# Kernel tuning notes

Measured on AMD Instinct MI355X. Metric: run time of the kernel, lower is better.

Reference implementation:

```python
import jax, jax.numpy as jnp
import numpy as np

FEAT_DIM = 2048
HID = 256
N = 1024
NUM_CLASSES = 16
BN_EPS = 1e-5


def _batchnorm(x, gamma, beta):
    # training-mode BatchNorm1d: per-batch mean, biased variance
    m = x.mean(axis=0)
    v = x.var(axis=0)
    return gamma * (x - m) / jnp.sqrt(v + BN_EPS) + beta


def setup_inputs() -> dict:
    key = jax.random.key(0)
    ks = jax.random.split(key, 12)
    s1 = 1.0 / np.sqrt(FEAT_DIM)
    s2 = 1.0 / np.sqrt(HID)
    s3 = 1.0 / np.sqrt(2 * HID)
    return {
        "features": jax.random.normal(ks[0], (N, FEAT_DIM), dtype=jnp.float32),
        "labels": jax.random.randint(ks[1], (N,), 0, NUM_CLASSES, dtype=jnp.int32),
        # semantic disentangler
        "W1": jax.random.normal(ks[2], (FEAT_DIM, HID), dtype=jnp.float32) * s1,
        "b1": jnp.zeros((HID,), jnp.float32),
        "g1": jnp.ones((HID,), jnp.float32),
        "bt1": jnp.zeros((HID,), jnp.float32),
        "W2": jax.random.normal(ks[3], (HID, HID), dtype=jnp.float32) * s2,
        "b2": jnp.zeros((HID,), jnp.float32),
        "g2": jnp.ones((HID,), jnp.float32),
        "bt2": jnp.zeros((HID,), jnp.float32),
        # edge network: Linear(2H -> H), Linear(H -> 1)
        "We1": jax.random.normal(ks[4], (2 * HID, HID), dtype=jnp.float32) * s3,
        "bwe1": jnp.zeros((HID,), jnp.float32),
        "We2": jax.random.normal(ks[5], (HID, 1), dtype=jnp.float32) * s2,
        "bwe2": jnp.zeros((1,), jnp.float32),
    }


def reference(features, labels, W1, b1, g1, bt1, W2, b2, g2, bt2,
              We1, bwe1, We2, bwe2):
    # semantic disentangler: (Linear -> BN -> ReLU) x2
    h = jax.nn.relu(_batchnorm(features @ W1 + b1, g1, bt1))
    di = jax.nn.relu(_batchnorm(h @ W2 + b2, g2, bt2))  # [N, H]

    # EdgeNetwork all-pairs: Linear on concat([f_i, f_j]) splits into two GEMMs
    hi = di @ We1[:HID]   # [N, H] contribution of node i (first half of concat)
    hj = di @ We1[HID:]   # [N, H] contribution of node j (second half)
    pair = jax.nn.relu(hi[:, None, :] + hj[None, :, :] + bwe1)  # [N, N, H]
    logits = pair @ We2[:, 0] + bwe2[0]                          # [N, N]
    same_label = labels[:, None] == labels[None, :]
    off_diag = ~jnp.eye(N, dtype=bool)
    edge_weights = jnp.where(same_label & off_diag,
                             jax.nn.sigmoid(logits), 0.0)        # [N, N]

    # update_node_features: f_i + sum_j w_ij f_j / sum_j w_ij (if wsum > 0)
    weighted_sum = edge_weights @ di                 # [N, H] (w_ii == 0)
    wsum = edge_weights.sum(axis=1, keepdims=True)   # [N, 1]
    denom = jnp.where(wsum > 0, wsum, 1.0)
    updated = di + jnp.where(wsum > 0, weighted_sum / denom, 0.0)
    return updated
```

## Files before the change

kernel.cpp:

```cpp
#include <hip/hip_runtime.h>
#include <math.h>

#define N_PTS 1024
#define HID   256
#define FEAT  2048

typedef short bf16x8 __attribute__((ext_vector_type(8)));
typedef float f32x4  __attribute__((ext_vector_type(4)));

__device__ inline ushort f2bf(float f) {
    union { float f; unsigned u; } v; v.f = f;
    unsigned r = v.u + 0x7fff + ((v.u >> 16) & 1);
    return (ushort)(r >> 16);
}

__global__ __launch_bounds__(256) void gemm_mfma(
    const float* __restrict__ A, const float* __restrict__ B,
    float* __restrict__ C, int lda, int ldb, int ldc, int kchunk)
{
    __shared__ ushort As[64 * 72];
    __shared__ ushort Bs[64 * 72];
    const int tid  = threadIdx.x;
    const int lane = tid & 63;
    const int wave = tid >> 6;
    const int wy = wave >> 1, wx = wave & 1;
    const int quad = lane >> 4, l16 = lane & 15;
    const int mBase = blockIdx.y * 64;
    const int nBase = blockIdx.x * 64;
    const int kBeg  = blockIdx.z * kchunk;

    f32x4 acc[2][2] = {};

    for (int ks = kBeg; ks < kBeg + kchunk; ks += 64) {
        #pragma unroll
        for (int p = 0; p < 4; p++) {
            const int c  = p * 256 + tid;
            const int r  = c >> 4;
            const int cq = c & 15;
            float4 av = *(const float4*)&A[(size_t)(mBase + r) * lda + ks + cq * 4];
            ushort4 ao;
            ao.x = f2bf(av.x); ao.y = f2bf(av.y);
            ao.z = f2bf(av.z); ao.w = f2bf(av.w);
            *(ushort4*)&As[r * 72 + cq * 4] = ao;
            float4 bv = *(const float4*)&B[(size_t)(ks + r) * ldb + nBase + cq * 4];
            Bs[(cq * 4 + 0) * 72 + r] = f2bf(bv.x);
            Bs[(cq * 4 + 1) * 72 + r] = f2bf(bv.y);
            Bs[(cq * 4 + 2) * 72 + r] = f2bf(bv.z);
            Bs[(cq * 4 + 3) * 72 + r] = f2bf(bv.w);
        }
        __syncthreads();
        #pragma unroll
        for (int kt = 0; kt < 64; kt += 32) {
            bf16x8 af[2], bfr[2];
            #pragma unroll
            for (int mi = 0; mi < 2; mi++)
                af[mi] = *(bf16x8*)&As[(wy * 32 + mi * 16 + l16) * 72 + kt + quad * 8];
            #pragma unroll
            for (int ni = 0; ni < 2; ni++)
                bfr[ni] = *(bf16x8*)&Bs[(wx * 32 + ni * 16 + l16) * 72 + kt + quad * 8];
            #pragma unroll
            for (int mi = 0; mi < 2; mi++)
                #pragma unroll
                for (int ni = 0; ni < 2; ni++)
                    acc[mi][ni] = __builtin_amdgcn_mfma_f32_16x16x32_bf16(
                        af[mi], bfr[ni], acc[mi][ni], 0, 0, 0);
        }
        __syncthreads();
    }
    #pragma unroll
    for (int mi = 0; mi < 2; mi++)
        #pragma unroll
        for (int ni = 0; ni < 2; ni++)
            #pragma unroll
            for (int e = 0; e < 4; e++) {
                const int gm = mBase + wy * 32 + mi * 16 + quad * 4 + e;
                const int gn = nBase + wx * 32 + ni * 16 + l16;
                unsafeAtomicAdd(&C[(size_t)gm * ldc + gn], acc[mi][ni][e]);
            }
}

__global__ __launch_bounds__(256) void colstats(
    const float* __restrict__ X, float* __restrict__ sum,
    float* __restrict__ sq, int rowsPerBlock)
{
    const int c = threadIdx.x;
    const int r0 = blockIdx.x * rowsPerBlock;
    float s = 0.f, q = 0.f;
    for (int r = r0; r < r0 + rowsPerBlock; ++r) {
        float v = X[r * HID + c];
        s += v;
        q = fmaf(v, v, q);
    }
    unsafeAtomicAdd(&sum[c], s);
    unsafeAtomicAdd(&sq[c], q);
}

__global__ __launch_bounds__(256) void bn_relu(
    const float* __restrict__ X, const float* __restrict__ sum,
    const float* __restrict__ sq, const float* __restrict__ g,
    const float* __restrict__ bt, float* __restrict__ Y)
{
    const int idx = blockIdx.x * 256 + threadIdx.x;
    const int cq = (idx & 63) * 4;
    float4 x = ((const float4*)X)[idx];
    float xv[4] = {x.x, x.y, x.z, x.w};
    float o[4];
    #pragma unroll
    for (int e = 0; e < 4; e++) {
        const int c = cq + e;
        float m   = sum[c] * (1.f / 1024.f);
        float var = fmaf(-m, m, sq[c] * (1.f / 1024.f));
        float rstd = rsqrtf(var + 1e-5f);
        o[e] = fmaxf(fmaf(g[c] * rstd, xv[e] - m, bt[c]), 0.f);
    }
    ((float4*)Y)[idx] = make_float4(o[0], o[1], o[2], o[3]);
}

__global__ __launch_bounds__(256) void pair_update(
    const float* __restrict__ di, const float* __restrict__ hi,
    const float* __restrict__ hj, const float* __restrict__ bwe1,
    const float* __restrict__ We2, const float* __restrict__ bwe2,
    const int* __restrict__ labels, float* __restrict__ out)
{
    __shared__ int   slab[N_PTS];
    __shared__ float sacc[4][HID];
    __shared__ float swsum[4];
    const int i = blockIdx.x;
    const int tid = threadIdx.x;
    const int lane = tid & 63;
    const int wave = tid >> 6;

    for (int t = tid; t < N_PTS; t += 256) slab[t] = labels[t];
    __syncthreads();

    const int myLab = slab[i];
    float4 hv_i = ((const float4*)(hi + (size_t)i * HID))[lane];
    float4 bw   = ((const float4*)bwe1)[lane];
    float4 w2   = ((const float4*)We2)[lane];
    const float hb0 = hv_i.x + bw.x, hb1 = hv_i.y + bw.y;
    const float hb2 = hv_i.z + bw.z, hb3 = hv_i.w + bw.w;
    const float b2 = bwe2[0];

    float a0 = 0.f, a1 = 0.f, a2 = 0.f, a3 = 0.f, wsum = 0.f;

    for (int chunk = wave * 64; chunk < N_PTS; chunk += 256) {
        const int j = chunk + lane;
        const bool match = (slab[j] == myLab) && (j != i);
        unsigned long long mask = __ballot(match);
        while (mask) {
            const int bpos = __builtin_ctzll(mask);
            mask &= mask - 1;
            const int jj = chunk + bpos;
            float4 hv = ((const float4*)(hj + (size_t)jj * HID))[lane];
            float p = fmaxf(hb0 + hv.x, 0.f) * w2.x
                    + fmaxf(hb1 + hv.y, 0.f) * w2.y
                    + fmaxf(hb2 + hv.z, 0.f) * w2.z
                    + fmaxf(hb3 + hv.w, 0.f) * w2.w;
            #pragma unroll
            for (int off = 1; off < 64; off <<= 1) p += __shfl_xor(p, off, 64);
            const float w = 1.f / (1.f + expf(-(p + b2)));
            float4 dv = ((const float4*)(di + (size_t)jj * HID))[lane];
            a0 = fmaf(w, dv.x, a0);
            a1 = fmaf(w, dv.y, a1);
            a2 = fmaf(w, dv.z, a2);
            a3 = fmaf(w, dv.w, a3);
            wsum += w;
        }
    }
    ((float4*)sacc[wave])[lane] = make_float4(a0, a1, a2, a3);
    if (lane == 0) swsum[wave] = wsum;
    __syncthreads();

    const float at = sacc[0][tid] + sacc[1][tid] + sacc[2][tid] + sacc[3][tid];
    const float wt = swsum[0] + swsum[1] + swsum[2] + swsum[3];
    const float dval = di[(size_t)i * HID + tid];
    out[(size_t)i * HID + tid] = dval + (wt > 0.f ? at / wt : 0.f);
}

extern "C" void kernel_launch(void* const* d_in, const int* in_sizes, int n_in,
                              void* d_out, int out_size, void* d_ws, size_t ws_size,
                              hipStream_t stream)
{
    const float* features = (const float*)d_in[0];
    const int*   labels   = (const int*)d_in[1];
    const float* W1   = (const float*)d_in[2];
    const float* g1   = (const float*)d_in[4];
    const float* bt1  = (const float*)d_in[5];
    const float* W2   = (const float*)d_in[6];
    const float* g2   = (const float*)d_in[8];
    const float* bt2  = (const float*)d_in[9];
    const float* We1  = (const float*)d_in[10];
    const float* bwe1 = (const float*)d_in[11];
    const float* We2  = (const float*)d_in[12];
    const float* bwe2 = (const float*)d_in[13];
    float* out = (float*)d_out;

    float* ws    = (float*)d_ws;
    float* x1    = ws;
    float* x2    = ws + 262144;
    float* hi    = ws + 524288;
    float* hj    = ws + 786432;
    float* stats = ws + 1048576;
    float* h     = ws + 1049600;
    float* di    = ws + 1311744;

    hipMemsetAsync(d_ws, 0, 1049600 * sizeof(float), stream);

    dim3 blk(256);
    gemm_mfma<<<dim3(4, 16, 8), blk, 0, stream>>>(features, W1, x1,
                                                  FEAT, HID, HID, 256);
    colstats<<<256, blk, 0, stream>>>(x1, stats, stats + 256, 4);
    bn_relu<<<256, blk, 0, stream>>>(x1, stats, stats + 256, g1, bt1, h);
    gemm_mfma<<<dim3(4, 16, 4), blk, 0, stream>>>(h, W2, x2,
                                                  HID, HID, HID, 64);
    colstats<<<256, blk, 0, stream>>>(x2, stats + 512, stats + 768, 4);
    bn_relu<<<256, blk, 0, stream>>>(x2, stats + 512, stats + 768, g2, bt2, di);
    gemm_mfma<<<dim3(4, 16, 4), blk, 0, stream>>>(di, We1, hi,
                                                  HID, HID, HID, 64);
    gemm_mfma<<<dim3(4, 16, 4), blk, 0, stream>>>(di, We1 + HID * HID, hj,
                                                  HID, HID, HID, 64);
    pair_update<<<N_PTS, blk, 0, stream>>>(di, hi, hj, bwe1, We2, bwe2,
                                           labels, out);
}
```

Measured before the change: 160.6 us.

## Fuse BN1 into GEMM2 with stats epilogue, merge edge GEMMs, restructure pair kernel

Folds the first BN+ReLU into the A-tile load of the second GEMM and computes column statistics for the second BN in that GEMM's epilogue. This removes the intermediate h buffer, one colstats launch, and the split-K atomics. The two edge GEMMs become a single launch, and the memset shrinks. The pair kernel now builds a compacted list of matching neighbours in shared memory and processes 16 pairs at once with 16-lane groups, replacing the per-match 64-lane reductions and giving more parallel work per block.

Measured after the change: 155.1 us. -3.4%, faster.

```diff
diff --git a/kernel.cpp b/kernel.cpp
--- a/kernel.cpp
+++ b/kernel.cpp
@@ -116,63 +116,258 @@
     ((float4*)Y)[idx] = make_float4(o[0], o[1], o[2], o[3]);
 }
 
-__global__ __launch_bounds__(256) void pair_update(
+__global__ __launch_bounds__(256) void gemm2_fused(
+    const float* __restrict__ A , const float* __restrict__ B ,
+    float* __restrict__ C ,
+    const float* __restrict__ sum1, const float* __restrict__ sq1,
+    const float* __restrict__ g1, const float* __restrict__ bt1,
+    float* __restrict__ sum2, float* __restrict__ sq2)
+{
+    __shared__ ushort As[64 * 72];
+    __shared__ ushort Bs[64 * 72];
+    __shared__ float sscale[HID];
+    __shared__ float sshift[HID];
+    __shared__ float csum[64];
+    __shared__ float csq[64];
+    const int tid  = threadIdx.x;
+    const int lane = tid & 63;
+    const int wave = tid >> 6;
+    const int wy = wave >> 1, wx = wave & 1;
+    const int quad = lane >> 4, l16 = lane & 15;
+    const int mBase = blockIdx.y * 64;
+    const int nBase = blockIdx.x * 64;
+
+    {
+        float m   = sum1[tid] * (1.f / 1024.f);
+        float var = fmaf(-m, m, sq1[tid] * (1.f / 1024.f));
+        float rstd = rsqrtf(var + 1e-5f);
+        float sc = g1[tid] * rstd;
+        sscale[tid] = sc;
+        sshift[tid] = fmaf(-m, sc, bt1[tid]);
+    }
+    if (tid < 64) { csum[tid] = 0.f; csq[tid] = 0.f; }
+    __syncthreads();
+
+    f32x4 acc[2][2] = {};
+    for (int ks = 0; ks < HID; ks += 64) {
+        #pragma unroll
+        for (int p = 0; p < 4; p++) {
+            const int c  = p * 256 + tid;
+            const int r  = c >> 4;
+            const int cq = c & 15;
+            const int k0 = ks + cq * 4;
+            float4 av = *(const float4*)&A[(size_t)(mBase + r) * HID + k0];
+            float v0 = fmaxf(fmaf(sscale[k0 + 0], av.x, sshift[k0 + 0]), 0.f);
+            float v1 = fmaxf(fmaf(sscale[k0 + 1], av.y, sshift[k0 + 1]), 0.f);
+            float v2 = fmaxf(fmaf(sscale[k0 + 2], av.z, sshift[k0 + 2]), 0.f);
+            float v3 = fmaxf(fmaf(sscale[k0 + 3], av.w, sshift[k0 + 3]), 0.f);
+            ushort4 ao;
+            ao.x = f2bf(v0); ao.y = f2bf(v1); ao.z = f2bf(v2); ao.w = f2bf(v3);
+            *(ushort4*)&As[r * 72 + cq * 4] = ao;
+            float4 bv = *(const float4*)&B[(size_t)(ks + r) * HID + nBase + cq * 4];
+            Bs[(cq * 4 + 0) * 72 + r] = f2bf(bv.x);
+            Bs[(cq * 4 + 1) * 72 + r] = f2bf(bv.y);
+            Bs[(cq * 4 + 2) * 72 + r] = f2bf(bv.z);
+            Bs[(cq * 4 + 3) * 72 + r] = f2bf(bv.w);
+        }
+        __syncthreads();
+        #pragma unroll
+        for (int kt = 0; kt < 64; kt += 32) {
+            bf16x8 af[2], bfr[2];
+            #pragma unroll
+            for (int mi = 0; mi < 2; mi++)
+                af[mi] = *(bf16x8*)&As[(wy * 32 + mi * 16 + l16) * 72 + kt + quad * 8];
+            #pragma unroll
+            for (int ni = 0; ni < 2; ni++)
+                bfr[ni] = *(bf16x8*)&Bs[(wx * 32 + ni * 16 + l16) * 72 + kt + quad * 8];
+            #pragma unroll
+            for (int mi = 0; mi < 2; mi++)
+                #pragma unroll
+                for (int ni = 0; ni < 2; ni++)
+                    acc[mi][ni] = __builtin_amdgcn_mfma_f32_16x16x32_bf16(
+                        af[mi], bfr[ni], acc[mi][ni], 0, 0, 0);
+        }
+        __syncthreads();
+    }
+
+    float s[2] = {0.f, 0.f}, q[2] = {0.f, 0.f};
+    #pragma unroll
+    for (int mi = 0; mi < 2; mi++)
+        #pragma unroll
+        for (int ni = 0; ni < 2; ni++)
+            #pragma unroll
+            for (int e = 0; e < 4; e++) {
+                const int gm = mBase + wy * 32 + mi * 16 + quad * 4 + e;
+                const int gn = nBase + wx * 32 + ni * 16 + l16;
+                float v = acc[mi][ni][e];
+                C[(size_t)gm * HID + gn] = v;
+                s[ni] += v;
+                q[ni] = fmaf(v, v, q[ni]);
+            }
+    #pragma unroll
+    for (int ni = 0; ni < 2; ni++) {
+        float sv = s[ni], qv = q[ni];
+        sv += __shfl_xor(sv, 16, 64); sv += __shfl_xor(sv, 32, 64);
+        qv += __shfl_xor(qv, 16, 64); qv += __shfl_xor(qv, 32, 64);
+        if (quad == 0) {
+            atomicAdd(&csum[wx * 32 + ni * 16 + l16], sv);
+            atomicAdd(&csq [wx * 32 + ni * 16 + l16], qv);
+        }
+    }
+    __syncthreads();
+    if (tid < 64) {
+        unsafeAtomicAdd(&sum2[nBase + tid], csum[tid]);
+        unsafeAtomicAdd(&sq2 [nBase + tid], csq[tid]);
+    }
+}
+
+__global__ __launch_bounds__(256) void gemm_dual(
+    const float* __restrict__ A, const float* __restrict__ B1,
+    const float* __restrict__ B2, float* __restrict__ C1, float* __restrict__ C2)
+{
+    __shared__ ushort As[64 * 72];
+    __shared__ ushort Bs[64 * 72];
+    const int tid  = threadIdx.x;
+    const int lane = tid & 63;
+    const int wave = tid >> 6;
+    const int wy = wave >> 1, wx = wave & 1;
+    const int quad = lane >> 4, l16 = lane & 15;
+    const int mBase = blockIdx.y * 64;
+    const int nBase = blockIdx.x * 64;
+    const float* B = (blockIdx.z >= 4) ? B2 : B1;
+    float*       C = (blockIdx.z >= 4) ? C2 : C1;
+    const int ks = (blockIdx.z & 3) * 64;
+
+    f32x4 acc[2][2] = {};
+    #pragma unroll
+    for (int p = 0; p < 4; p++) {
+        const int c  = p * 256 + tid;
+        const int r  = c >> 4;
+        const int cq = c & 15;
+        float4 av = *(const float4*)&A[(size_t)(mBase + r) * HID + ks + cq * 4];
+        ushort4 ao;
+        ao.x = f2bf(av.x); ao.y = f2bf(av.y);
+        ao.z = f2bf(av.z); ao.w = f2bf(av.w);
+        *(ushort4*)&As[r * 72 + cq * 4] = ao;
+        float4 bv = *(const float4*)&B[(size_t)(ks + r) * HID + nBase + cq * 4];
+        Bs[(cq * 4 + 0) * 72 + r] = f2bf(bv.x);
+        Bs[(cq * 4 + 1) * 72 + r] = f2bf(bv.y);
+        Bs[(cq * 4 + 2) * 72 + r] = f2bf(bv.z);
+        Bs[(cq * 4 + 3) * 72 + r] = f2bf(bv.w);
+    }
+    __syncthreads();
+    #pragma unroll
+    for (int kt = 0; kt < 64; kt += 32) {
+        bf16x8 af[2], bfr[2];
+        #pragma unroll
+        for (int mi = 0; mi < 2; mi++)
+            af[mi] = *(bf16x8*)&As[(wy * 32 + mi * 16 + l16) * 72 + kt + quad * 8];
+        #pragma unroll
+        for (int ni = 0; ni < 2; ni++)
+            bfr[ni] = *(bf16x8*)&Bs[(wx * 32 + ni * 16 + l16) * 72 + kt + quad * 8];
+        #pragma unroll
+        for (int mi = 0; mi < 2; mi++)
+            #pragma unroll
+            for (int ni = 0; ni < 2; ni++)
+                acc[mi][ni] = __builtin_amdgcn_mfma_f32_16x16x32_bf16(
+                    af[mi], bfr[ni], acc[mi][ni], 0, 0, 0);
+    }
+    #pragma unroll
+    for (int mi = 0; mi < 2; mi++)
+        #pragma unroll
+        for (int ni = 0; ni < 2; ni++)
+            #pragma unroll
+            for (int e = 0; e < 4; e++) {
+                const int gm = mBase + wy * 32 + mi * 16 + quad * 4 + e;
+                const int gn = nBase + wx * 32 + ni * 16 + l16;
+                unsafeAtomicAdd(&C[(size_t)gm * HID + gn], acc[mi][ni][e]);
+            }
+}
+
+__global__ __launch_bounds__(256) void pair_update2(
     const float* __restrict__ di, const float* __restrict__ hi,
     const float* __restrict__ hj, const float* __restrict__ bwe1,
     const float* __restrict__ We2, const float* __restrict__ bwe2,
     const int* __restrict__ labels, float* __restrict__ out)
 {
     __shared__ int   slab[N_PTS];
-    __shared__ float sacc[4][HID];
-    __shared__ float swsum[4];
-    const int i = blockIdx.x;
+    __shared__ int   list[N_PTS];
+    __shared__ int   cnt;
+    __shared__ float sacc[16][HID];
+    __shared__ float swsum[16];
+    const int i   = blockIdx.x;
     const int tid = threadIdx.x;
-    const int lane = tid & 63;
-    const int wave = tid >> 6;
-
+    const int pid = tid >> 4;
+    const int l16 = tid & 15;
+
+    if (tid == 0) cnt = 0;
     for (int t = tid; t < N_PTS; t += 256) slab[t] = labels[t];
     __syncthreads();
-
     const int myLab = slab[i];
-    float4 hv_i = ((const float4*)(hi + (size_t)i * HID))[lane];
-    float4 bw   = ((const float4*)bwe1)[lane];
-    float4 w2   = ((const float4*)We2)[lane];
-    const float hb0 = hv_i.x + bw.x, hb1 = hv_i.y + bw.y;
-    const float hb2 = hv_i.z + bw.z, hb3 = hv_i.w + bw.w;
+    for (int t = tid; t < N_PTS; t += 256)
+        if (slab[t] == myLab && t != i) list[atomicAdd(&cnt, 1)] = t;
+    __syncthreads();
+    const int n = cnt;
+
+    const float4* hip4 = (const float4*)(hi + (size_t)i * HID) + l16 * 4;
+    const float4* bw4  = (const float4*)bwe1 + l16 * 4;
+    const float4* w24  = (const float4*)We2  + l16 * 4;
+    float4 hb[4], w2[4];
+    #pragma unroll
+    for (int s = 0; s < 4; s++) {
+        float4 a = hip4[s], b = bw4[s];
+        hb[s] = make_float4(a.x + b.x, a.y + b.y, a.z + b.z, a.w + b.w);
+        w2[s] = w24[s];
+    }
     const float b2 = bwe2[0];
 
-    float a0 = 0.f, a1 = 0.f, a2 = 0.f, a3 = 0.f, wsum = 0.f;
-
-    for (int chunk = wave * 64; chunk < N_PTS; chunk += 256) {
-        const int j = chunk + lane;
-        const bool match = (slab[j] == myLab) && (j != i);
-        unsigned long long mask = __ballot(match);
-        while (mask) {
-            const int bpos = __builtin_ctzll(mask);
-            mask &= mask - 1;
-            const int jj = chunk + bpos;
-            float4 hv = ((const float4*)(hj + (size_t)jj * HID))[lane];
-            float p = fmaxf(hb0 + hv.x, 0.f) * w2.x
-                    + fmaxf(hb1 + hv.y, 0.f) * w2.y
-                    + fmaxf(hb2 + hv.z, 0.f) * w2.z
-                    + fmaxf(hb3 + hv.w, 0.f) * w2.w;
-            #pragma unroll
-            for (int off = 1; off < 64; off <<= 1) p += __shfl_xor(p, off, 64);
-            const float w = 1.f / (1.f + expf(-(p + b2)));
-            float4 dv = ((const float4*)(di + (size_t)jj * HID))[lane];
-            a0 = fmaf(w, dv.x, a0);
-            a1 = fmaf(w, dv.y, a1);
-            a2 = fmaf(w, dv.z, a2);
-            a3 = fmaf(w, dv.w, a3);
-            wsum += w;
-        }
-    }
-    ((float4*)sacc[wave])[lane] = make_float4(a0, a1, a2, a3);
-    if (lane == 0) swsum[wave] = wsum;
-    __syncthreads();
-
-    const float at = sacc[0][tid] + sacc[1][tid] + sacc[2][tid] + sacc[3][tid];
-    const float wt = swsum[0] + swsum[1] + swsum[2] + swsum[3];
+    float4 acc[4] = {};
+    float wloc = 0.f;
+    const int rounds = (n + 15) >> 4;
+    for (int r = 0; r < rounds; ++r) {
+        const int idx = r * 16 + pid;
+        const bool valid = idx < n;
+        const int jj = valid ? list[idx] : i;
+        const float4* hv4 = (const float4*)(hj + (size_t)jj * HID) + l16 * 4;
+        float4 hv[4];
+        #pragma unroll
+        for (int s = 0; s < 4; s++) hv[s] = hv4[s];
+        float p = 0.f;
+        #pragma unroll
+        for (int s = 0; s < 4; s++) {
+            p = fmaf(fmaxf(hb[s].x + hv[s].x, 0.f), w2[s].x, p);
+            p = fmaf(fmaxf(hb[s].y + hv[s].y, 0.f), w2[s].y, p);
+            p = fmaf(fmaxf(hb[s].z + hv[s].z, 0.f), w2[s].z, p);
+            p = fmaf(fmaxf(hb[s].w + hv[s].w, 0.f), w2[s].w, p);
+        }
+        p += __shfl_xor(p, 1, 64);
+        p += __shfl_xor(p, 2, 64);
+        p += __shfl_xor(p, 4, 64);
+        p += __shfl_xor(p, 8, 64);
+        const float w = valid ? 1.f / (1.f + expf(-(p + b2))) : 0.f;
+        const float4* dv4 = (const float4*)(di + (size_t)jj * HID) + l16 * 4;
+        #pragma unroll
+        for (int s = 0; s < 4; s++) {
+            float4 d = dv4[s];
+            acc[s].x = fmaf(w, d.x, acc[s].x);
+            acc[s].y = fmaf(w, d.y, acc[s].y);
+            acc[s].z = fmaf(w, d.z, acc[s].z);
+            acc[s].w = fmaf(w, d.w, acc[s].w);
+        }
+        if (l16 == 0) wloc += w;
+    }
+    #pragma unroll
+    for (int s = 0; s < 4; s++)
+        ((float4*)&sacc[pid][l16 * 16])[s] = acc[s];
+    if (l16 == 0) swsum[pid] = wloc;
+    __syncthreads();
+
+    float at = 0.f;
+    #pragma unroll
+    for (int g = 0; g < 16; g++) at += sacc[g][tid];
+    float wt = 0.f;
+    #pragma unroll
+    for (int g = 0; g < 16; g++) wt += swsum[g];
     const float dval = di[(size_t)i * HID + tid];
     out[(size_t)i * HID + tid] = dval + (wt > 0.f ? at / wt : 0.f);
 }
@@ -197,28 +392,24 @@
 
     float* ws    = (float*)d_ws;
     float* x1    = ws;
-    float* x2    = ws + 262144;
-    float* hi    = ws + 524288;
-    float* hj    = ws + 786432;
-    float* stats = ws + 1048576;
-    float* h     = ws + 1049600;
-    float* di    = ws + 1311744;
-
-    hipMemsetAsync(d_ws, 0, 1049600 * sizeof(float), stream);
+    float* hi    = ws + 262144;
+    float* hj    = ws + 524288;
+    float* stats = ws + 786432;
+    float* x2    = ws + 787456;
+    float* di    = ws + 1049600;
+
+    hipMemsetAsync(d_ws, 0, 787456 * sizeof(float), stream);
 
     dim3 blk(256);
     gemm_mfma<<<dim3(4, 16, 8), blk, 0, stream>>>(features, W1, x1,
                                                   FEAT, HID, HID, 256);
     colstats<<<256, blk, 0, stream>>>(x1, stats, stats + 256, 4);
-    bn_relu<<<256, blk, 0, stream>>>(x1, stats, stats + 256, g1, bt1, h);
-    gemm_mfma<<<dim3(4, 16, 4), blk, 0, stream>>>(h, W2, x2,
-                                                  HID, HID, HID, 64);
-    colstats<<<256, blk, 0, stream>>>(x2, stats + 512, stats + 768, 4);
+    gemm2_fused<<<dim3(4, 16, 1), blk, 0, stream>>>(x1, W2, x2,
+                                                    stats, stats + 256, g1, bt1,
+                                                    stats + 512, stats + 768);
     bn_relu<<<256, blk, 0, stream>>>(x2, stats + 512, stats + 768, g2, bt2, di);
-    gemm_mfma<<<dim3(4, 16, 4), blk, 0, stream>>>(di, We1, hi,
-                                                  HID, HID, HID, 64);
-    gemm_mfma<<<dim3(4, 16, 4), blk, 0, stream>>>(di, We1 + HID * HID, hj,
-                                                  HID, HID, HID, 64);
-    pair_update<<<N_PTS, blk, 0, stream>>>(di, hi, hj, bwe1, We2, bwe2,
-                                           labels, out);
-}
+    gemm_dual<<<dim3(4, 16, 8), blk, 0, stream>>>(di, We1, We1 + HID * HID,
+                                                  hi, hj);
+    pair_update2<<<N_PTS, blk, 0, stream>>>(di, hi, hj, bwe1, We2, bwe2,
+                                            labels, out);
+}
```
